# Performance work log

Hardware: AMD Instinct MI355X
Metric: run time of the kernel (lower is better)

The kernel has to match this reference:

```python
import jax, jax.numpy as jnp
import numpy as np

N_HEAD = 16
D_MODEL = 1024
D_K = D_MODEL // N_HEAD  # 64, also d_v
B, S = 8, 1024


def setup_inputs() -> dict:
    key = jax.random.key(0)
    ks = jax.random.split(key, 7)
    sc = 1.0 / np.sqrt(D_MODEL)
    return {
        "q": jax.random.normal(ks[0], (B, S, D_MODEL), jnp.float32),
        "k": jax.random.normal(ks[1], (B, S, D_MODEL), jnp.float32),
        "v": jax.random.normal(ks[2], (B, S, D_MODEL), jnp.float32),
        "Wq": jax.random.normal(ks[3], (N_HEAD, D_MODEL, D_K), jnp.float32) * sc,
        "Wk": jax.random.normal(ks[4], (N_HEAD, D_MODEL, D_K), jnp.float32) * sc,
        "Wv": jax.random.normal(ks[5], (D_MODEL, D_K), jnp.float32) * sc,  # shared across heads
        "Wo": jax.random.normal(ks[6], (D_K, D_MODEL), jnp.float32) * (1.0 / np.sqrt(D_K)),
    }


def reference(q, k, v, Wq, Wk, Wv, Wo):
    # Faithful to original: qs, ks, vs are ALL projected from q (k, v args unused),
    # and Wv is shared across all heads. Dropout is identity (rate 0 / eval).
    qs = jnp.einsum('bsd,hdk->hbsk', q, Wq)          # [H,B,S,dk]
    kk = jnp.einsum('bsd,hdk->hbsk', q, Wk)          # [H,B,S,dk]
    vs = jnp.einsum('bsd,dk->bsk', q, Wv)            # [B,S,dv] shared
    scale = 1.0 / jnp.sqrt(jnp.asarray(D_K, jnp.float32))
    scores = jnp.einsum('hbik,hbjk->hbij', qs, kk) * scale  # [H,B,S,S]
    attn = jax.nn.softmax(scores, axis=-1)
    head = jnp.einsum('hbij,bjk->hbik', attn, vs)    # [H,B,S,dv]
    pooled = jnp.mean(head, axis=0)                  # mean over heads, not concat
    out = jnp.einsum('bsk,kd->bsd', pooled, Wo)      # [B,S,d_model]
    return (out, attn)
```

## Files before the change

### kernel.cpp

```cpp
#include <hip/hip_runtime.h>
#include <hip/hip_bf16.h>
#include <stdint.h>

#define NC 2112

typedef __attribute__((ext_vector_type(8))) short bf16x8;
typedef __attribute__((ext_vector_type(4))) float f32x4;

static __device__ __forceinline__ unsigned short f2bf(float f) {
  uint32_t u = __builtin_bit_cast(uint32_t, f);
  u += 0x7FFFu + ((u >> 16) & 1u);
  return (unsigned short)(u >> 16);
}
static __device__ __forceinline__ float bf2f(unsigned short u) {
  return __builtin_bit_cast(float, ((uint32_t)u) << 16);
}
static __device__ __forceinline__ void gload16(const unsigned short* g, unsigned short* l) {
  __builtin_amdgcn_global_load_lds((const __attribute__((address_space(1))) void*)g,
                                   (__attribute__((address_space(3))) void*)l, 16, 0, 0);
}

__global__ void k_convert_q(const float* __restrict__ q, unsigned short* __restrict__ qbf) {
  int i = blockIdx.x * blockDim.x + threadIdx.x;
  float4 v = ((const float4*)q)[i];
  ushort4 o;
  o.x = f2bf(v.x); o.y = f2bf(v.y); o.z = f2bf(v.z); o.w = f2bf(v.w);
  ((ushort4*)qbf)[i] = o;
}

__global__ void k_build_wcatT(const float* __restrict__ Wq, const float* __restrict__ Wk,
                              const float* __restrict__ Wv, unsigned short* __restrict__ wt) {
  int t = blockIdx.x * blockDim.x + threadIdx.x;
  int c = t >> 7;
  int k0 = (t & 127) << 3;
  unsigned short o[8];
#pragma unroll
  for (int i = 0; i < 8; ++i) {
    int k = k0 + i;
    float v;
    if (c < 1024)      v = Wq[((size_t)(c >> 6) * 1024 + k) * 64 + (c & 63)];
    else if (c < 2048) v = Wk[((size_t)((c - 1024) >> 6) * 1024 + k) * 64 + (c & 63)];
    else               v = Wv[(size_t)k * 64 + (c - 2048)];
    o[i] = f2bf(v);
  }
  *(ushort4*)&wt[(size_t)c * 1024 + k0]     = *(ushort4*)&o[0];
  *(ushort4*)&wt[(size_t)c * 1024 + k0 + 4] = *(ushort4*)&o[4];
}

__global__ __launch_bounds__(256) void k_gemm(const unsigned short* __restrict__ A,
                                              const unsigned short* __restrict__ Bt,
                                              unsigned short* __restrict__ C) {
  __shared__ unsigned short As[128 * 32];
  __shared__ unsigned short Bs[128 * 32];
  const int tn = blockIdx.x, tm = blockIdx.y;
  const int rowBase = tm * 128, colBase = tn * 128;
  const int t = threadIdx.x;
  const int wave = t >> 6, lane = t & 63;
  const int wm = wave >> 1, wn = wave & 1;
  const int l15 = lane & 15, l4 = lane >> 4;
  f32x4 acc[4][4] = {};
  for (int kt = 0; kt < 1024; kt += 32) {
#pragma unroll
    for (int i = 0; i < 2; ++i) {
      int e = (t + i * 256) * 8;
      int r = e >> 5, c = e & 31;
      gload16(&A[(size_t)(rowBase + r) * 1024 + kt + c], &As[e]);
      int rb = colBase + r; rb = rb < NC ? rb : (NC - 1);
      gload16(&Bt[(size_t)rb * 1024 + kt + c], &Bs[e]);
    }
    __syncthreads();
    bf16x8 af[4], bfr[4];
#pragma unroll
    for (int m = 0; m < 4; ++m) af[m] = *(const bf16x8*)&As[(wm * 64 + m * 16 + l15) * 32 + l4 * 8];
#pragma unroll
    for (int n = 0; n < 4; ++n) bfr[n] = *(const bf16x8*)&Bs[(wn * 64 + n * 16 + l15) * 32 + l4 * 8];
#pragma unroll
    for (int m = 0; m < 4; ++m)
#pragma unroll
      for (int n = 0; n < 4; ++n)
        acc[m][n] = __builtin_amdgcn_mfma_f32_16x16x32_bf16(af[m], bfr[n], acc[m][n], 0, 0, 0);
    __syncthreads();
  }
#pragma unroll
  for (int m = 0; m < 4; ++m)
#pragma unroll
    for (int n = 0; n < 4; ++n) {
      int col = colBase + wn * 64 + n * 16 + l15;
      if (col < NC) {
        int row0 = rowBase + wm * 64 + m * 16 + l4 * 4;
#pragma unroll
        for (int i = 0; i < 4; ++i)
          C[(size_t)(row0 + i) * NC + col] = f2bf(acc[m][n][i]);
      }
    }
}

__global__ void k_transpose_v(const unsigned short* __restrict__ G, unsigned short* __restrict__ vst) {
  int t = blockIdx.x * blockDim.x + threadIdx.x;
  int d = t & 63;
  int j = (t >> 6) & 1023;
  int b = t >> 16;
  vst[(size_t)(b * 64 + d) * 1024 + j] = G[(size_t)(b * 1024 + j) * NC + 2048 + d];
}

__global__ __launch_bounds__(512, 4) void k_attn(const unsigned short* __restrict__ G,
                                                 const unsigned short* __restrict__ vst,
                                                 float* __restrict__ attn,
                                                 float* __restrict__ head) {
  __shared__ unsigned short SP[32][1032];
  const int qt = blockIdx.x, b = blockIdx.y, h = blockIdx.z;
  const int t = threadIdx.x, wave = t >> 6, lane = t & 63;
  const int l15 = lane & 15, l4 = lane >> 4;

  const unsigned short* Gb = G + (size_t)b * 1024 * NC;

  bf16x8 qf[2][2];
#pragma unroll
  for (int m = 0; m < 2; ++m)
#pragma unroll
    for (int ks = 0; ks < 2; ++ks)
      qf[m][ks] = *(const bf16x8*)&Gb[(size_t)(qt * 32 + m * 16 + l15) * NC + h * 64 + ks * 32 + l4 * 8];

  const float scale = 0.125f;
#pragma unroll
  for (int half = 0; half < 2; ++half) {
    bf16x8 kf[4][2];
#pragma unroll
    for (int kt = 0; kt < 4; ++kt) {
      int k0 = wave * 128 + (half * 4 + kt) * 16;
#pragma unroll
      for (int ks = 0; ks < 2; ++ks)
        kf[kt][ks] = *(const bf16x8*)&Gb[(size_t)(k0 + l15) * NC + 1024 + h * 64 + ks * 32 + l4 * 8];
    }
#pragma unroll
    for (int kt = 0; kt < 4; ++kt) {
      int k0 = wave * 128 + (half * 4 + kt) * 16;
      f32x4 s0 = {}, s1 = {};
      s0 = __builtin_amdgcn_mfma_f32_16x16x32_bf16(qf[0][0], kf[kt][0], s0, 0, 0, 0);
      s0 = __builtin_amdgcn_mfma_f32_16x16x32_bf16(qf[0][1], kf[kt][1], s0, 0, 0, 0);
      s1 = __builtin_amdgcn_mfma_f32_16x16x32_bf16(qf[1][0], kf[kt][0], s1, 0, 0, 0);
      s1 = __builtin_amdgcn_mfma_f32_16x16x32_bf16(qf[1][1], kf[kt][1], s1, 0, 0, 0);
#pragma unroll
      for (int i = 0; i < 4; ++i) {
        SP[l4 * 4 + i][k0 + l15]      = f2bf(s0[i] * scale);
        SP[16 + l4 * 4 + i][k0 + l15] = f2bf(s1[i] * scale);
      }
    }
  }
  __syncthreads();

  size_t attn_base = ((size_t)(h * 8 + b) * 1024 + (size_t)qt * 32) * 1024;
#pragma unroll
  for (int rr = 0; rr < 4; ++rr) {
    int row = wave * 4 + rr;
    float sv[16];
#pragma unroll
    for (int c = 0; c < 2; ++c) {
      uint4 u = *(const uint4*)&SP[row][c * 512 + lane * 8];
      sv[c*8+0] = bf2f((unsigned short)(u.x & 0xFFFF));
      sv[c*8+1] = bf2f((unsigned short)(u.x >> 16));
      sv[c*8+2] = bf2f((unsigned short)(u.y & 0xFFFF));
      sv[c*8+3] = bf2f((unsigned short)(u.y >> 16));
      sv[c*8+4] = bf2f((unsigned short)(u.z & 0xFFFF));
      sv[c*8+5] = bf2f((unsigned short)(u.z >> 16));
      sv[c*8+6] = bf2f((unsigned short)(u.w & 0xFFFF));
      sv[c*8+7] = bf2f((unsigned short)(u.w >> 16));
    }
    float mx = sv[0];
#pragma unroll
    for (int i = 1; i < 16; ++i) mx = fmaxf(mx, sv[i]);
#pragma unroll
    for (int off = 32; off > 0; off >>= 1) mx = fmaxf(mx, __shfl_xor(mx, off));
    float sum = 0.f;
#pragma unroll
    for (int i = 0; i < 16; ++i) { sv[i] = __expf(sv[i] - mx); sum += sv[i]; }
#pragma unroll
    for (int off = 32; off > 0; off >>= 1) sum += __shfl_xor(sum, off);
    float inv = 1.0f / sum;
#pragma unroll
    for (int c = 0; c < 2; ++c) {
      float4 p0 = {sv[c*8+0]*inv, sv[c*8+1]*inv, sv[c*8+2]*inv, sv[c*8+3]*inv};
      float4 p1 = {sv[c*8+4]*inv, sv[c*8+5]*inv, sv[c*8+6]*inv, sv[c*8+7]*inv};
      float* ab = &attn[attn_base + (size_t)row * 1024 + c * 512 + lane * 8];
      *(float4*)ab = p0;
      *(float4*)(ab + 4) = p1;
      uint4 o;
      o.x = (uint32_t)f2bf(p0.x) | ((uint32_t)f2bf(p0.y) << 16);
      o.y = (uint32_t)f2bf(p0.z) | ((uint32_t)f2bf(p0.w) << 16);
      o.z = (uint32_t)f2bf(p1.x) | ((uint32_t)f2bf(p1.y) << 16);
      o.w = (uint32_t)f2bf(p1.z) | ((uint32_t)f2bf(p1.w) << 16);
      *(uint4*)&SP[row][c * 512 + lane * 8] = o;
    }
  }
  __syncthreads();

  const int wm = wave >> 2, wn = wave & 3;
  const unsigned short* vb = vst + ((size_t)b * 64 + wn * 16 + l15) * 1024;
  const unsigned short* pr = &SP[wm * 16 + l15][0];
  f32x4 o0 = {}, o1 = {};
#pragma unroll 8
  for (int jt = 0; jt < 32; jt += 2) {
    bf16x8 pa0 = *(const bf16x8*)&pr[jt * 32 + l4 * 8];
    bf16x8 bv0 = *(const bf16x8*)&vb[jt * 32 + l4 * 8];
    o0 = __builtin_amdgcn_mfma_f32_16x16x32_bf16(pa0, bv0, o0, 0, 0, 0);
    bf16x8 pa1 = *(const bf16x8*)&pr[(jt + 1) * 32 + l4 * 8];
    bf16x8 bv1 = *(const bf16x8*)&vb[(jt + 1) * 32 + l4 * 8];
    o1 = __builtin_amdgcn_mfma_f32_16x16x32_bf16(pa1, bv1, o1, 0, 0, 0);
  }
  f32x4 oacc = o0 + o1;
  float* hb = head + (((size_t)(h * 8 + b) * 1024) + qt * 32 + wm * 16) * 64 + wn * 16;
#pragma unroll
  for (int i = 0; i < 4; ++i)
    hb[(size_t)(l4 * 4 + i) * 64 + l15] = oacc[i];
}

__global__ void k_pooled(const float* __restrict__ head, float* __restrict__ pooled) {
  int i = blockIdx.x * blockDim.x + threadIdx.x;
  int r = i >> 4;
  int k4 = (i & 15) * 4;
  float4 acc = {0.f, 0.f, 0.f, 0.f};
#pragma unroll
  for (int h = 0; h < 16; ++h) {
    float4 v = *(const float4*)&head[((size_t)h * 8192 + r) * 64 + k4];
    acc.x += v.x; acc.y += v.y; acc.z += v.z; acc.w += v.w;
  }
  const float s = 1.0f / 16.0f;
  acc.x *= s; acc.y *= s; acc.z *= s; acc.w *= s;
  *(float4*)&pooled[(size_t)r * 64 + k4] = acc;
}

__global__ __launch_bounds__(256) void k_final(const float* __restrict__ pooled,
                                               const float* __restrict__ Wo,
                                               float* __restrict__ out) {
  __shared__ float Ps[64][64];
  __shared__ float Ws[64][132];
  const int dt = blockIdx.x, rt = blockIdx.y;
  const int r0 = rt * 64, d0 = dt * 128;
  const int t = threadIdx.x;
#pragma unroll
  for (int j = 0; j < 4; ++j) {
    int e = t + j * 256;
    int r = e >> 4, k4 = (e & 15) * 4;
    *(float4*)&Ps[r][k4] = *(const float4*)&pooled[(size_t)(r0 + r) * 64 + k4];
  }
#pragma unroll
  for (int j = 0; j < 8; ++j) {
    int e = t + j * 256;
    int k = e >> 5, c4 = (e & 31) * 4;
    *(float4*)&Ws[k][c4] = *(const float4*)&Wo[(size_t)k * 1024 + d0 + c4];
  }
  __syncthreads();
  const int ty = t >> 4, tx = t & 15;
  float acc[4][8] = {};
  for (int k = 0; k < 64; ++k) {
    float a_[4], b_[8];
#pragma unroll
    for (int i = 0; i < 4; ++i) a_[i] = Ps[ty * 4 + i][k];
#pragma unroll
    for (int j = 0; j < 8; ++j) b_[j] = Ws[k][tx * 8 + j];
#pragma unroll
    for (int i = 0; i < 4; ++i)
#pragma unroll
      for (int j = 0; j < 8; ++j) acc[i][j] += a_[i] * b_[j];
  }
#pragma unroll
  for (int i = 0; i < 4; ++i) {
    float4 v0 = {acc[i][0], acc[i][1], acc[i][2], acc[i][3]};
    float4 v1 = {acc[i][4], acc[i][5], acc[i][6], acc[i][7]};
    size_t o = (size_t)(r0 + ty * 4 + i) * 1024 + d0 + tx * 8;
    *(float4*)&out[o]     = v0;
    *(float4*)&out[o + 4] = v1;
  }
}

extern "C" void kernel_launch(void* const* d_in, const int* in_sizes, int n_in,
                              void* d_out, int out_size, void* d_ws, size_t ws_size,
                              hipStream_t stream) {
  const float* q  = (const float*)d_in[0];
  const float* Wq = (const float*)d_in[3];
  const float* Wk = (const float*)d_in[4];
  const float* Wv = (const float*)d_in[5];
  const float* Wo = (const float*)d_in[6];

  char* ws = (char*)d_ws;
  unsigned short* qbf   = (unsigned short*)(ws + 0);
  unsigned short* wcatT = (unsigned short*)(ws + 16777216);
  unsigned short* G     = (unsigned short*)(ws + 21102592);
  unsigned short* vst   = (unsigned short*)(ws + 55705600);
  float*          head  = (float*)(ws + 56754176);
  float*          pooled= (float*)(ws + 90308608);

  float* out  = (float*)d_out;
  float* attn = out + (size_t)8 * 1024 * 1024;

  hipLaunchKernelGGL(k_convert_q,   dim3(8192),       dim3(256), 0, stream, q, qbf);
  hipLaunchKernelGGL(k_build_wcatT, dim3(1056),       dim3(256), 0, stream, Wq, Wk, Wv, wcatT);
  hipLaunchKernelGGL(k_gemm,        dim3(17, 64),     dim3(256), 0, stream, qbf, wcatT, G);
  hipLaunchKernelGGL(k_transpose_v, dim3(2048),       dim3(256), 0, stream, G, vst);
  hipLaunchKernelGGL(k_attn,        dim3(32, 8, 16),  dim3(512), 0, stream, G, vst, attn, head);
  hipLaunchKernelGGL(k_pooled,      dim3(512),        dim3(256), 0, stream, head, pooled);
  hipLaunchKernelGGL(k_final,       dim3(8, 128),     dim3(256), 0, stream, pooled, Wo, out);
}
```

Before: 390.9 us.

## Fuse V transpose into GEMM, drop softmax max pass, fuse pooling into output GEMM

The GEMM epilogue now writes the V columns straight into the transposed layout, which removes the separate transpose kernel. Attention computes exp of the scores without subtracting the row max and takes row sums from per-wave partial sums. It defers normalization of the PV product to a final scale, writes attn with nontemporal stores, and drops the second sync and the re-quantization of P. The head-mean pooling is folded into the output projection kernel, and both GEMM and attention grids are remapped through an XCD-aware block swizzle. Skipping the max subtraction risks overflow for large scores, and the unnormalized bf16 P slightly changes numerics.

```diff
diff --git a/kernel.cpp b/kernel.cpp
--- a/kernel.cpp
+++ b/kernel.cpp
@@ -49,10 +49,13 @@
 
 __global__ __launch_bounds__(256) void k_gemm(const unsigned short* __restrict__ A,
                                               const unsigned short* __restrict__ Bt,
-                                              unsigned short* __restrict__ C) {
+                                              unsigned short* __restrict__ C,
+                                              unsigned short* __restrict__ vst) {
   __shared__ unsigned short As[128 * 32];
   __shared__ unsigned short Bs[128 * 32];
-  const int tn = blockIdx.x, tm = blockIdx.y;
+  const int L = blockIdx.x;
+  const int wi = (L & 7) * 136 + (L >> 3);
+  const int tn = wi % 17, tm = wi / 17;
   const int rowBase = tm * 128, colBase = tn * 128;
   const int t = threadIdx.x;
   const int wave = t >> 6, lane = t & 63;
@@ -86,21 +89,20 @@
 #pragma unroll
     for (int n = 0; n < 4; ++n) {
       int col = colBase + wn * 64 + n * 16 + l15;
-      if (col < NC) {
-        int row0 = rowBase + wm * 64 + m * 16 + l4 * 4;
+      int row0 = rowBase + wm * 64 + m * 16 + l4 * 4;
+      if (col < 2048) {
 #pragma unroll
         for (int i = 0; i < 4; ++i)
           C[(size_t)(row0 + i) * NC + col] = f2bf(acc[m][n][i]);
+      } else if (col < NC) {
+        int d = col - 2048;
+#pragma unroll
+        for (int i = 0; i < 4; ++i) {
+          int rg = row0 + i;
+          vst[((size_t)(rg >> 10) * 64 + d) * 1024 + (rg & 1023)] = f2bf(acc[m][n][i]);
+        }
       }
     }
-}
-
-__global__ void k_transpose_v(const unsigned short* __restrict__ G, unsigned short* __restrict__ vst) {
-  int t = blockIdx.x * blockDim.x + threadIdx.x;
-  int d = t & 63;
-  int j = (t >> 6) & 1023;
-  int b = t >> 16;
-  vst[(size_t)(b * 64 + d) * 1024 + j] = G[(size_t)(b * 1024 + j) * NC + 2048 + d];
 }
 
 __global__ __launch_bounds__(512, 4) void k_attn(const unsigned short* __restrict__ G,
@@ -108,7 +110,10 @@
                                                  float* __restrict__ attn,
                                                  float* __restrict__ head) {
   __shared__ unsigned short SP[32][1032];
-  const int qt = blockIdx.x, b = blockIdx.y, h = blockIdx.z;
+  __shared__ float rs[32][8];
+  const int L = blockIdx.x;
+  const int wi = (L & 7) * 512 + (L >> 3);
+  const int qt = wi & 31, b = (wi >> 5) & 7, h = wi >> 8;
   const int t = threadIdx.x, wave = t >> 6, lane = t & 63;
   const int l15 = lane & 15, l4 = lane >> 4;
 
@@ -122,6 +127,7 @@
       qf[m][ks] = *(const bf16x8*)&Gb[(size_t)(qt * 32 + m * 16 + l15) * NC + h * 64 + ks * 32 + l4 * 8];
 
   const float scale = 0.125f;
+  float psum[2][4] = {};
 #pragma unroll
   for (int half = 0; half < 2; ++half) {
     bf16x8 kf[4][2];
@@ -142,59 +148,70 @@
       s1 = __builtin_amdgcn_mfma_f32_16x16x32_bf16(qf[1][1], kf[kt][1], s1, 0, 0, 0);
 #pragma unroll
       for (int i = 0; i < 4; ++i) {
-        SP[l4 * 4 + i][k0 + l15]      = f2bf(s0[i] * scale);
-        SP[16 + l4 * 4 + i][k0 + l15] = f2bf(s1[i] * scale);
+        unsigned short u0 = f2bf(__expf(s0[i] * scale));
+        unsigned short u1 = f2bf(__expf(s1[i] * scale));
+        SP[l4 * 4 + i][k0 + l15]      = u0;
+        SP[16 + l4 * 4 + i][k0 + l15] = u1;
+        psum[0][i] += bf2f(u0);
+        psum[1][i] += bf2f(u1);
       }
     }
   }
+#pragma unroll
+  for (int off = 1; off < 16; off <<= 1)
+#pragma unroll
+    for (int m = 0; m < 2; ++m)
+#pragma unroll
+      for (int i = 0; i < 4; ++i)
+        psum[m][i] += __shfl_xor(psum[m][i], off);
+  if (l15 == 0) {
+#pragma unroll
+    for (int m = 0; m < 2; ++m)
+#pragma unroll
+      for (int i = 0; i < 4; ++i)
+        rs[m * 16 + l4 * 4 + i][wave] = psum[m][i];
+  }
   __syncthreads();
 
-  size_t attn_base = ((size_t)(h * 8 + b) * 1024 + (size_t)qt * 32) * 1024;
+  const int wm = wave >> 2, wn = wave & 3;
+  float winv[4], pinv[4];
 #pragma unroll
   for (int rr = 0; rr < 4; ++rr) {
     int row = wave * 4 + rr;
-    float sv[16];
+    float4 a = *(const float4*)&rs[row][0];
+    float4 c = *(const float4*)&rs[row][4];
+    winv[rr] = 1.0f / (a.x + a.y + a.z + a.w + c.x + c.y + c.z + c.w);
+  }
+#pragma unroll
+  for (int i = 0; i < 4; ++i) {
+    int row = wm * 16 + l4 * 4 + i;
+    float4 a = *(const float4*)&rs[row][0];
+    float4 c = *(const float4*)&rs[row][4];
+    pinv[i] = 1.0f / (a.x + a.y + a.z + a.w + c.x + c.y + c.z + c.w);
+  }
+
+  size_t attn_base = ((size_t)(h * 8 + b) * 1024 + (size_t)qt * 32) * 1024;
+#pragma unroll
+  for (int rr = 0; rr < 4; ++rr) {
+    int row = wave * 4 + rr;
+    float inv = winv[rr];
 #pragma unroll
     for (int c = 0; c < 2; ++c) {
       uint4 u = *(const uint4*)&SP[row][c * 512 + lane * 8];
-      sv[c*8+0] = bf2f((unsigned short)(u.x & 0xFFFF));
-      sv[c*8+1] = bf2f((unsigned short)(u.x >> 16));
-      sv[c*8+2] = bf2f((unsigned short)(u.y & 0xFFFF));
-      sv[c*8+3] = bf2f((unsigned short)(u.y >> 16));
-      sv[c*8+4] = bf2f((unsigned short)(u.z & 0xFFFF));
-      sv[c*8+5] = bf2f((unsigned short)(u.z >> 16));
-      sv[c*8+6] = bf2f((unsigned short)(u.w & 0xFFFF));
-      sv[c*8+7] = bf2f((unsigned short)(u.w >> 16));
-    }
-    float mx = sv[0];
-#pragma unroll
-    for (int i = 1; i < 16; ++i) mx = fmaxf(mx, sv[i]);
-#pragma unroll
-    for (int off = 32; off > 0; off >>= 1) mx = fmaxf(mx, __shfl_xor(mx, off));
-    float sum = 0.f;
-#pragma unroll
-    for (int i = 0; i < 16; ++i) { sv[i] = __expf(sv[i] - mx); sum += sv[i]; }
-#pragma unroll
-    for (int off = 32; off > 0; off >>= 1) sum += __shfl_xor(sum, off);
-    float inv = 1.0f / sum;
-#pragma unroll
-    for (int c = 0; c < 2; ++c) {
-      float4 p0 = {sv[c*8+0]*inv, sv[c*8+1]*inv, sv[c*8+2]*inv, sv[c*8+3]*inv};
-      float4 p1 = {sv[c*8+4]*inv, sv[c*8+5]*inv, sv[c*8+6]*inv, sv[c*8+7]*inv};
+      f32x4 p0 = {bf2f((unsigned short)(u.x & 0xFFFF)) * inv,
+                  bf2f((unsigned short)(u.x >> 16)) * inv,
+                  bf2f((unsigned short)(u.y & 0xFFFF)) * inv,
+                  bf2f((unsigned short)(u.y >> 16)) * inv};
+      f32x4 p1 = {bf2f((unsigned short)(u.z & 0xFFFF)) * inv,
+                  bf2f((unsigned short)(u.z >> 16)) * inv,
+                  bf2f((unsigned short)(u.w & 0xFFFF)) * inv,
+                  bf2f((unsigned short)(u.w >> 16)) * inv};
       float* ab = &attn[attn_base + (size_t)row * 1024 + c * 512 + lane * 8];
-      *(float4*)ab = p0;
-      *(float4*)(ab + 4) = p1;
-      uint4 o;
-      o.x = (uint32_t)f2bf(p0.x) | ((uint32_t)f2bf(p0.y) << 16);
-      o.y = (uint32_t)f2bf(p0.z) | ((uint32_t)f2bf(p0.w) << 16);
-      o.z = (uint32_t)f2bf(p1.x) | ((uint32_t)f2bf(p1.y) << 16);
-      o.w = (uint32_t)f2bf(p1.z) | ((uint32_t)f2bf(p1.w) << 16);
-      *(uint4*)&SP[row][c * 512 + lane * 8] = o;
-    }
-  }
-  __syncthreads();
-
-  const int wm = wave >> 2, wn = wave & 3;
+      __builtin_nontemporal_store(p0, (f32x4*)ab);
+      __builtin_nontemporal_store(p1, (f32x4*)(ab + 4));
+    }
+  }
+
   const unsigned short* vb = vst + ((size_t)b * 64 + wn * 16 + l15) * 1024;
   const unsigned short* pr = &SP[wm * 16 + l15][0];
   f32x4 o0 = {}, o1 = {};
@@ -207,69 +224,63 @@
     bf16x8 bv1 = *(const bf16x8*)&vb[(jt + 1) * 32 + l4 * 8];
     o1 = __builtin_amdgcn_mfma_f32_16x16x32_bf16(pa1, bv1, o1, 0, 0, 0);
   }
-  f32x4 oacc = o0 + o1;
   float* hb = head + (((size_t)(h * 8 + b) * 1024) + qt * 32 + wm * 16) * 64 + wn * 16;
 #pragma unroll
   for (int i = 0; i < 4; ++i)
-    hb[(size_t)(l4 * 4 + i) * 64 + l15] = oacc[i];
-}
-
-__global__ void k_pooled(const float* __restrict__ head, float* __restrict__ pooled) {
-  int i = blockIdx.x * blockDim.x + threadIdx.x;
-  int r = i >> 4;
-  int k4 = (i & 15) * 4;
-  float4 acc = {0.f, 0.f, 0.f, 0.f};
-#pragma unroll
-  for (int h = 0; h < 16; ++h) {
-    float4 v = *(const float4*)&head[((size_t)h * 8192 + r) * 64 + k4];
-    acc.x += v.x; acc.y += v.y; acc.z += v.z; acc.w += v.w;
-  }
-  const float s = 1.0f / 16.0f;
-  acc.x *= s; acc.y *= s; acc.z *= s; acc.w *= s;
-  *(float4*)&pooled[(size_t)r * 64 + k4] = acc;
-}
-
-__global__ __launch_bounds__(256) void k_final(const float* __restrict__ pooled,
+    hb[(size_t)(l4 * 4 + i) * 64 + l15] = (o0[i] + o1[i]) * pinv[i];
+}
+
+__global__ __launch_bounds__(256) void k_final(const float* __restrict__ head,
                                                const float* __restrict__ Wo,
                                                float* __restrict__ out) {
-  __shared__ float Ps[64][64];
+  __shared__ float Ps[32][68];
   __shared__ float Ws[64][132];
-  const int dt = blockIdx.x, rt = blockIdx.y;
-  const int r0 = rt * 64, d0 = dt * 128;
+  const int rt = blockIdx.x;
+  const int r0 = rt * 32;
   const int t = threadIdx.x;
 #pragma unroll
-  for (int j = 0; j < 4; ++j) {
+  for (int j = 0; j < 2; ++j) {
     int e = t + j * 256;
     int r = e >> 4, k4 = (e & 15) * 4;
-    *(float4*)&Ps[r][k4] = *(const float4*)&pooled[(size_t)(r0 + r) * 64 + k4];
-  }
-#pragma unroll
-  for (int j = 0; j < 8; ++j) {
-    int e = t + j * 256;
-    int k = e >> 5, c4 = (e & 31) * 4;
-    *(float4*)&Ws[k][c4] = *(const float4*)&Wo[(size_t)k * 1024 + d0 + c4];
-  }
-  __syncthreads();
+    float4 acc = {0.f, 0.f, 0.f, 0.f};
+#pragma unroll
+    for (int hh = 0; hh < 16; ++hh) {
+      float4 v = *(const float4*)&head[((size_t)hh * 8192 + r0 + r) * 64 + k4];
+      acc.x += v.x; acc.y += v.y; acc.z += v.z; acc.w += v.w;
+    }
+    const float s = 1.0f / 16.0f;
+    Ps[r][k4] = acc.x * s; Ps[r][k4 + 1] = acc.y * s;
+    Ps[r][k4 + 2] = acc.z * s; Ps[r][k4 + 3] = acc.w * s;
+  }
   const int ty = t >> 4, tx = t & 15;
-  float acc[4][8] = {};
-  for (int k = 0; k < 64; ++k) {
-    float a_[4], b_[8];
-#pragma unroll
-    for (int i = 0; i < 4; ++i) a_[i] = Ps[ty * 4 + i][k];
-#pragma unroll
-    for (int j = 0; j < 8; ++j) b_[j] = Ws[k][tx * 8 + j];
-#pragma unroll
-    for (int i = 0; i < 4; ++i)
-#pragma unroll
-      for (int j = 0; j < 8; ++j) acc[i][j] += a_[i] * b_[j];
-  }
-#pragma unroll
-  for (int i = 0; i < 4; ++i) {
-    float4 v0 = {acc[i][0], acc[i][1], acc[i][2], acc[i][3]};
-    float4 v1 = {acc[i][4], acc[i][5], acc[i][6], acc[i][7]};
-    size_t o = (size_t)(r0 + ty * 4 + i) * 1024 + d0 + tx * 8;
-    *(float4*)&out[o]     = v0;
-    *(float4*)&out[o + 4] = v1;
+  for (int dt = 0; dt < 8; ++dt) {
+    int d0 = dt * 128;
+#pragma unroll
+    for (int j = 0; j < 8; ++j) {
+      int e = t + j * 256;
+      int k = e >> 5, c4 = (e & 31) * 4;
+      *(float4*)&Ws[k][c4] = *(const float4*)&Wo[(size_t)k * 1024 + d0 + c4];
+    }
+    __syncthreads();
+    float acc[2][8] = {};
+    for (int k = 0; k < 64; ++k) {
+      float a0 = Ps[ty * 2][k], a1 = Ps[ty * 2 + 1][k];
+      float4 b0 = *(const float4*)&Ws[k][tx * 8];
+      float4 b1 = *(const float4*)&Ws[k][tx * 8 + 4];
+      acc[0][0] += a0 * b0.x; acc[0][1] += a0 * b0.y; acc[0][2] += a0 * b0.z; acc[0][3] += a0 * b0.w;
+      acc[0][4] += a0 * b1.x; acc[0][5] += a0 * b1.y; acc[0][6] += a0 * b1.z; acc[0][7] += a0 * b1.w;
+      acc[1][0] += a1 * b0.x; acc[1][1] += a1 * b0.y; acc[1][2] += a1 * b0.z; acc[1][3] += a1 * b0.w;
+      acc[1][4] += a1 * b1.x; acc[1][5] += a1 * b1.y; acc[1][6] += a1 * b1.z; acc[1][7] += a1 * b1.w;
+    }
+#pragma unroll
+    for (int i = 0; i < 2; ++i) {
+      float4 v0 = {acc[i][0], acc[i][1], acc[i][2], acc[i][3]};
+      float4 v1 = {acc[i][4], acc[i][5], acc[i][6], acc[i][7]};
+      size_t o = (size_t)(r0 + ty * 2 + i) * 1024 + d0 + tx * 8;
+      *(float4*)&out[o]     = v0;
+      *(float4*)&out[o + 4] = v1;
+    }
+    __syncthreads();
   }
 }
 
@@ -288,16 +299,13 @@
   unsigned short* G     = (unsigned short*)(ws + 21102592);
   unsigned short* vst   = (unsigned short*)(ws + 55705600);
   float*          head  = (float*)(ws + 56754176);
-  float*          pooled= (float*)(ws + 90308608);
 
   float* out  = (float*)d_out;
   float* attn = out + (size_t)8 * 1024 * 1024;
 
-  hipLaunchKernelGGL(k_convert_q,   dim3(8192),       dim3(256), 0, stream, q, qbf);
-  hipLaunchKernelGGL(k_build_wcatT, dim3(1056),       dim3(256), 0, stream, Wq, Wk, Wv, wcatT);
-  hipLaunchKernelGGL(k_gemm,        dim3(17, 64),     dim3(256), 0, stream, qbf, wcatT, G);
-  hipLaunchKernelGGL(k_transpose_v, dim3(2048),       dim3(256), 0, stream, G, vst);
-  hipLaunchKernelGGL(k_attn,        dim3(32, 8, 16),  dim3(512), 0, stream, G, vst, attn, head);
-  hipLaunchKernelGGL(k_pooled,      dim3(512),        dim3(256), 0, stream, head, pooled);
-  hipLaunchKernelGGL(k_final,       dim3(8, 128),     dim3(256), 0, stream, pooled, Wo, out);
-}
+  hipLaunchKernelGGL(k_convert_q,   dim3(8192), dim3(256), 0, stream, q, qbf);
+  hipLaunchKernelGGL(k_build_wcatT, dim3(1056), dim3(256), 0, stream, Wq, Wk, Wv, wcatT);
+  hipLaunchKernelGGL(k_gemm,        dim3(1088), dim3(256), 0, stream, qbf, wcatT, G, vst);
+  hipLaunchKernelGGL(k_attn,        dim3(4096), dim3(512), 0, stream, G, vst, attn, head);
+  hipLaunchKernelGGL(k_final,       dim3(256),  dim3(256), 0, stream, head, Wo, out);
+}
```

After: 354.9 us. -9.2%, faster.
